# Kernel optimization log

Hardware: AMD Instinct MI355X
Metric: run time of the kernel (lower is better)

## Reference

```python
import jax, jax.numpy as jnp
import numpy as np

D_IN = 1024
D_OUT = 1024
N_HEADS = 16
D_K = D_OUT // N_HEADS
ROPE_THETA = 10000.0


def setup_inputs() -> dict:
    key = jax.random.key(0)
    ks = jax.random.split(key, 5)
    x = jax.random.normal(ks[0], (2, 2048, D_IN), dtype=jnp.float32)
    token_positions = jnp.arange(2048, dtype=jnp.int32)
    scale = 0.02
    wq = jax.random.normal(ks[1], (D_OUT, D_IN), dtype=jnp.float32) * scale
    wk = jax.random.normal(ks[2], (D_OUT, D_IN), dtype=jnp.float32) * scale
    wv = jax.random.normal(ks[3], (D_OUT, D_IN), dtype=jnp.float32) * scale
    wo = jax.random.normal(ks[4], (D_OUT, D_OUT), dtype=jnp.float32) * scale
    return {"x": x, "token_positions": token_positions, "wq": wq, "wk": wk, "wv": wv, "wo": wo}


def _rope(x, token_positions):
    # x: [..., S, d_k]; token_positions: [S]
    d_k = x.shape[-1]
    idx = jnp.arange(d_k)
    k = idx // 2
    # thetas[i, j] = pos_i / theta^(2*(j//2)/d_k)
    angles = token_positions[:, None].astype(x.dtype) / jnp.power(
        jnp.asarray(ROPE_THETA, x.dtype), 2.0 * k.astype(x.dtype) / d_k
    )  # [S, d_k]
    cos = jnp.cos(angles)
    sin = jnp.sin(angles) * jnp.where(idx % 2 == 0, -1.0, 1.0).astype(x.dtype)
    pair_swaps = idx + jnp.where(idx % 2 == 0, 1, -1)  # swap even/odd pairs
    return x * cos + x[..., pair_swaps] * sin


def _forward(x, token_positions, wq, wk, wv, wo):
    B, S, _ = x.shape
    # fused QKV projection (same math as concat + split)
    q = jnp.einsum("bsd,od->bso", x, wq)
    k = jnp.einsum("bsd,od->bso", x, wk)
    v = jnp.einsum("bsd,od->bso", x, wv)
    # split heads: [B, S, H*dk] -> [B, H, S, dk]
    split = lambda t: t.reshape(B, S, N_HEADS, D_K).transpose(0, 2, 1, 3)
    q, k, v = split(q), split(k), split(v)
    q = _rope(q, token_positions)
    k = _rope(k, token_positions)
    scores = jnp.einsum("bhqd,bhkd->bhqk", q, k) / jnp.sqrt(jnp.asarray(D_K, x.dtype))
    causal = jnp.tril(jnp.ones((S, S), dtype=bool))
    scores = jnp.where(causal, scores, -jnp.inf)
    probs = jax.nn.softmax(scores, axis=-1)
    ctx = jnp.einsum("bhqk,bhkd->bhqd", probs, v)
    merged = ctx.transpose(0, 2, 1, 3).reshape(B, S, D_OUT)
    return jnp.einsum("bsm,om->bso", merged, wo)


def reference(x, token_positions, wq, wk, wv, wo):
    return _forward(x, token_positions, wq, wk, wv, wo)
```

## Files before the change

### kernel.cpp

```cpp
#include <hip/hip_runtime.h>

#define D_MODEL 1024
#define SEQ     2048
#define BATCH   2
#define NHEADS  16
#define DK      64
#define NROWS   (BATCH*SEQ)

typedef unsigned short u16;
typedef __bf16 bf16x8 __attribute__((ext_vector_type(8)));
typedef float  f32x4  __attribute__((ext_vector_type(4)));

__device__ __forceinline__ u16 f2bf(float f) {
    union { float f; unsigned u; } v; v.f = f;
    unsigned u = v.u;
    u += 0x7fffu + ((u >> 16) & 1);
    return (u16)(u >> 16);
}
__device__ __forceinline__ float bf2f(u16 h) {
    union { unsigned u; float f; } v; v.u = ((unsigned)h) << 16;
    return v.f;
}
__device__ __forceinline__ unsigned cvtpk_bf16(float lo, float hi) {
    unsigned r;
    asm("v_cvt_pk_bf16_f32 %0, %1, %2" : "=v"(r) : "v"(lo), "v"(hi));
    return r;
}

__device__ __forceinline__ void gload_lds16(const u16* g, u16* l) {
    __builtin_amdgcn_global_load_lds(
        (const __attribute__((address_space(1))) void*)g,
        (__attribute__((address_space(3))) void*)l, 16, 0, 0);
}

__global__ void cvt_bf16_all(const float* __restrict__ x,
                             const float* __restrict__ w0, const float* __restrict__ w1,
                             const float* __restrict__ w2, const float* __restrict__ w3,
                             u16* __restrict__ xb, u16* __restrict__ wb) {
    int i = blockIdx.x * blockDim.x + threadIdx.x;
    int row = i >> 8;
    int c   = (i & 255) * 4;
    const float* src; u16* dst;
    if (row < 4096) {
        src = x + (size_t)row * 1024;
        dst = xb + (size_t)row * 1024;
    } else {
        int r2 = row - 4096;
        int ws = r2 >> 10;
        int rr = r2 & 1023;
        const float* wsrc = ws == 0 ? w0 : ws == 1 ? w1 : ws == 2 ? w2 : w3;
        src = wsrc + (size_t)rr * 1024;
        dst = wb + ((size_t)ws << 20) + (size_t)rr * 1024;
    }
    float4 v = *(const float4*)(src + c);
    uint2 o;
    o.x = (unsigned)f2bf(v.x) | ((unsigned)f2bf(v.y) << 16);
    o.y = (unsigned)f2bf(v.z) | ((unsigned)f2bf(v.w) << 16);
    *(uint2*)(dst + c) = o;
}

__global__ __launch_bounds__(256) void gemm_qkv_p(
    const u16* __restrict__ A, const u16* __restrict__ W,
    u16* __restrict__ Qp, u16* __restrict__ Kp, u16* __restrict__ Vt)
{
    __shared__ __align__(16) u16 Ash[128 * 32];
    __shared__ __align__(16) u16 Bsh[128 * 32];

    const int m0  = blockIdx.x * 128;
    const int sel = blockIdx.y >> 3;
    const int n0  = (blockIdx.y & 7) * 128;
    const u16* B = W + ((size_t)sel << 20);
    const int tid = threadIdx.x;
    const int lane = tid & 63;
    const int w    = tid >> 6;
    const int wr = w >> 1, wc = w & 1;
    const int fr = lane & 15;
    const int fk = (lane >> 4) * 8;
    const int rsub = lane >> 2;
    const int csub = (lane & 3) * 8;

    f32x4 acc[4][4];
#pragma unroll
    for (int i = 0; i < 4; ++i)
#pragma unroll
        for (int j = 0; j < 4; ++j) acc[i][j] = (f32x4){0.f, 0.f, 0.f, 0.f};

    for (int k0 = 0; k0 < 1024; k0 += 32) {
        __syncthreads();
        const u16* Ab = A + (size_t)(m0 + 16 * w + rsub) * 1024 + k0 + csub;
        const u16* Bb = B + (size_t)(n0 + 16 * w + rsub) * 1024 + k0 + csub;
#pragma unroll
        for (int half = 0; half < 2; ++half) {
            size_t ro = (size_t)(half * 64) * 1024;
            int lo = (half * 64 + 16 * w) * 32;
            gload_lds16(Ab + ro, &Ash[lo]);
            gload_lds16(Bb + ro, &Bsh[lo]);
        }
        __syncthreads();

        bf16x8 ah[4], bh[4];
#pragma unroll
        for (int i = 0; i < 4; ++i)
            ah[i] = *(const bf16x8*)&Ash[(wr * 64 + i * 16 + fr) * 32 + fk];
#pragma unroll
        for (int j = 0; j < 4; ++j)
            bh[j] = *(const bf16x8*)&Bsh[(wc * 64 + j * 16 + fr) * 32 + fk];
#pragma unroll
        for (int i = 0; i < 4; ++i)
#pragma unroll
            for (int j = 0; j < 4; ++j)
                acc[i][j] = __builtin_amdgcn_mfma_f32_16x16x32_bf16(ah[i], bh[j], acc[i][j], 0, 0, 0);
    }

    const int r0 = (lane >> 4) * 4;
#pragma unroll
    for (int i = 0; i < 4; ++i) {
#pragma unroll
        for (int j = 0; j < 4; ++j) {
            int col = n0 + wc * 64 + j * 16 + fr;
#pragma unroll
            for (int r = 0; r < 4; ++r) {
                int row = m0 + wr * 64 + i * 16 + r0 + r;
                u16 v = f2bf(acc[i][j][r]);
                if (sel == 0)      Qp[(size_t)row * 1024 + col] = v;
                else if (sel == 1) Kp[(size_t)row * 1024 + col] = v;
                else               Vt[(size_t)col * NROWS + row] = v;
            }
        }
    }
}

__global__ __launch_bounds__(256) void gemm_out_p(
    const u16* __restrict__ A, const u16* __restrict__ B, float* __restrict__ Cout)
{
    __shared__ __align__(16) u16 Ash[128 * 32];
    __shared__ __align__(16) u16 Bsh[128 * 32];

    const int m0 = blockIdx.x * 128;
    const int n0 = blockIdx.y * 128;
    const int tid = threadIdx.x;
    const int lane = tid & 63;
    const int w    = tid >> 6;
    const int wr = w >> 1, wc = w & 1;
    const int fr = lane & 15;
    const int fk = (lane >> 4) * 8;
    const int rsub = lane >> 2;
    const int csub = (lane & 3) * 8;

    f32x4 acc[4][4];
#pragma unroll
    for (int i = 0; i < 4; ++i)
#pragma unroll
        for (int j = 0; j < 4; ++j) acc[i][j] = (f32x4){0.f, 0.f, 0.f, 0.f};

    for (int k0 = 0; k0 < 1024; k0 += 32) {
        __syncthreads();
        const u16* Ab = A + (size_t)(m0 + 16 * w + rsub) * 1024 + k0 + csub;
        const u16* Bb = B + (size_t)(n0 + 16 * w + rsub) * 1024 + k0 + csub;
#pragma unroll
        for (int half = 0; half < 2; ++half) {
            size_t ro = (size_t)(half * 64) * 1024;
            int lo = (half * 64 + 16 * w) * 32;
            gload_lds16(Ab + ro, &Ash[lo]);
            gload_lds16(Bb + ro, &Bsh[lo]);
        }
        __syncthreads();

        bf16x8 ah[4], bh[4];
#pragma unroll
        for (int i = 0; i < 4; ++i)
            ah[i] = *(const bf16x8*)&Ash[(wr * 64 + i * 16 + fr) * 32 + fk];
#pragma unroll
        for (int j = 0; j < 4; ++j)
            bh[j] = *(const bf16x8*)&Bsh[(wc * 64 + j * 16 + fr) * 32 + fk];
#pragma unroll
        for (int i = 0; i < 4; ++i)
#pragma unroll
            for (int j = 0; j < 4; ++j)
                acc[i][j] = __builtin_amdgcn_mfma_f32_16x16x32_bf16(ah[i], bh[j], acc[i][j], 0, 0, 0);
    }

    const int r0 = (lane >> 4) * 4;
#pragma unroll
    for (int i = 0; i < 4; ++i) {
#pragma unroll
        for (int j = 0; j < 4; ++j) {
            int col = n0 + wc * 64 + j * 16 + fr;
#pragma unroll
            for (int r = 0; r < 4; ++r)
                Cout[(size_t)(m0 + wr * 64 + i * 16 + r0 + r) * 1024 + col] = acc[i][j][r];
        }
    }
}

__global__ void rope_plain(u16* __restrict__ qk, const int* __restrict__ pos) {
    int i = blockIdx.x * blockDim.x + threadIdx.x;
    int p = i & 511;
    int n = i >> 9;
    int s = n & 2047;
    int k = p & 31;
    int h = p >> 5;
    size_t base = (size_t)n * 1024 + h * DK + 2 * k;
    unsigned v = *(const unsigned*)&qk[base];
    float x0 = bf2f((u16)(v & 0xffff));
    float x1 = bf2f((u16)(v >> 16));
    float ang = (float)pos[s] * expf((float)k * -0.28782313662425575f);
    float c = cosf(ang), sn = sinf(ang);
    float qs = (n < 4096) ? 0.18033688011112042f : 1.0f;
    c *= qs; sn *= qs;
    float y0 = x0 * c - x1 * sn;
    float y1 = x1 * c + x0 * sn;
    *(unsigned*)&qk[base] = (unsigned)f2bf(y0) | ((unsigned)f2bf(y1) << 16);
}

__global__ __launch_bounds__(512, 4) void attn_v7(
    const u16* __restrict__ Qp, const u16* __restrict__ Kp, const u16* __restrict__ Vt,
    u16* __restrict__ Op, float* __restrict__ mlbuf)
{
    const int slot = 39 - (int)blockIdx.x;
    const int h = blockIdx.y, b = blockIdx.z;
    int g, rr;
    if (slot < 4)       { g = 0; rr = slot; }
    else if (slot < 12) { g = 1; rr = slot - 4; }
    else if (slot < 24) { g = 2; rr = slot - 12; }
    else                { g = 3; rr = slot - 24; }
    const int qq  = rr / (g + 1);
    const int qt2 = 4 * g + qq;
    const int c   = rr - qq * (g + 1);

    const int tid  = threadIdx.x;
    const int lane = tid & 63;
    const int w    = tid >> 6;
    const int fr = lane & 15;
    const int fg = lane >> 4;
    const int bS = b * SEQ;
    const int hd = h * DK;
    const int qbase = qt2 * 128 + 16 * w;
    const int ntk = 2 * qt2 + 2;
    const int kt0 = 8 * c;
    const int kt1 = min(8 * c + 8, ntk);

    __shared__ __align__(16) u16 Kl[2][64 * 64];
    __shared__ __align__(16) u16 Vl[2][64 * 64];
    __shared__ __align__(16) u16 Plds[8][16][72];

    const int srow = 8 * w + (lane >> 3);
    const int scol = (((lane & 7) ^ (lane >> 3)) * 8);
    const int swz  = (fr & 7) * 8;

    const u16* qrow = Qp + (size_t)(bS + qbase + fr) * 1024 + hd;
    bf16x8 qf0 = *(const bf16x8*)(qrow + fg * 8);
    bf16x8 qf1 = *(const bf16x8*)(qrow + 32 + fg * 8);

    f32x4 o[4];
#pragma unroll
    for (int j = 0; j < 4; ++j) o[j] = (f32x4){0.f, 0.f, 0.f, 0.f};
    float mrow = -1e30f, lrow = 0.f;

#define STAGE(BUF, KT) do { \
    int kb_ = (KT) * 64; \
    gload_lds16(Kp + (size_t)(bS + kb_ + srow) * 1024 + hd + scol, &Kl[BUF][(8 * w) * 64]); \
    gload_lds16(Vt + (size_t)(hd + srow) * NROWS + bS + kb_ + scol, &Vl[BUF][(8 * w) * 64]); \
} while (0)

    STAGE(0, kt0);
    __syncthreads();

    int cur = 0;
    for (int kt = kt0; kt < kt1; ++kt) {
        if (kt + 1 < kt1) STAGE(cur ^ 1, kt + 1);
        const int k0 = kt * 64;
        if (k0 <= qbase + 15) {
            bf16x8 kf[4][2];
#pragma unroll
            for (int t = 0; t < 4; ++t) {
                const u16* kr = &Kl[cur][(16 * t + fr) * 64];
                kf[t][0] = *(const bf16x8*)(kr + ((fg * 8) ^ swz));
                kf[t][1] = *(const bf16x8*)(kr + (((4 + fg) * 8) ^ swz));
            }
            f32x4 sc4[4];
#pragma unroll
            for (int t = 0; t < 4; ++t) {
                f32x4 a = (f32x4){0.f, 0.f, 0.f, 0.f};
                a = __builtin_amdgcn_mfma_f32_16x16x32_bf16(kf[t][0], qf0, a, 0, 0, 0);
                a = __builtin_amdgcn_mfma_f32_16x16x32_bf16(kf[t][1], qf1, a, 0, 0, 0);
                sc4[t] = a;
            }
            float p[4][4];
#pragma unroll
            for (int t = 0; t < 4; ++t)
#pragma unroll
                for (int r = 0; r < 4; ++r) p[t][r] = sc4[t][r];
            if (k0 + 63 > qbase) {
#pragma unroll
                for (int t = 0; t < 4; ++t)
#pragma unroll
                    for (int r = 0; r < 4; ++r)
                        if (k0 + 16 * t + 4 * fg + r > qbase + fr) p[t][r] = -1e30f;
            }
            float a0 = fmaxf(fmaxf(p[0][0], p[0][1]), fmaxf(p[0][2], p[0][3]));
            float a1 = fmaxf(fmaxf(p[1][0], p[1][1]), fmaxf(p[1][2], p[1][3]));
            float a2 = fmaxf(fmaxf(p[2][0], p[2][1]), fmaxf(p[2][2], p[2][3]));
            float a3 = fmaxf(fmaxf(p[3][0], p[3][1]), fmaxf(p[3][2], p[3][3]));
            float mx = fmaxf(fmaxf(a0, a1), fmaxf(a2, a3));
            mx = fmaxf(mx, __shfl_xor(mx, 16));
            mx = fmaxf(mx, __shfl_xor(mx, 32));
            float scf = 1.0f;
            if (!__all(mx <= mrow + 8.0f)) {
                float mnew = fmaxf(mrow, mx);
                scf = exp2f(mrow - mnew);
                float s0 = __shfl(scf, 4 * fg);
                float s1 = __shfl(scf, 4 * fg + 1);
                float s2 = __shfl(scf, 4 * fg + 2);
                float s3 = __shfl(scf, 4 * fg + 3);
#pragma unroll
                for (int j = 0; j < 4; ++j) {
                    o[j][0] *= s0; o[j][1] *= s1; o[j][2] *= s2; o[j][3] *= s3;
                }
                mrow = mnew;
            }
            float rs = 0.f;
#pragma unroll
            for (int t = 0; t < 4; ++t)
#pragma unroll
                for (int r = 0; r < 4; ++r) {
                    p[t][r] = exp2f(p[t][r] - mrow);
                    rs += p[t][r];
                }
            rs += __shfl_xor(rs, 16);
            rs += __shfl_xor(rs, 32);
            lrow = lrow * scf + rs;
#pragma unroll
            for (int t = 0; t < 4; ++t) {
                uint2 pk;
                pk.x = cvtpk_bf16(p[t][0], p[t][1]);
                pk.y = cvtpk_bf16(p[t][2], p[t][3]);
                *(uint2*)&Plds[w][fr][16 * t + 4 * fg] = pk;
            }
            bf16x8 pf0 = *(const bf16x8*)&Plds[w][fr][fg * 8];
            bf16x8 pf1 = *(const bf16x8*)&Plds[w][fr][32 + fg * 8];
#pragma unroll
            for (int j = 0; j < 4; ++j) {
                const u16* vr = &Vl[cur][(16 * j + fr) * 64];
                bf16x8 v0 = *(const bf16x8*)(vr + ((fg * 8) ^ swz));
                bf16x8 v1 = *(const bf16x8*)(vr + (((4 + fg) * 8) ^ swz));
                o[j] = __builtin_amdgcn_mfma_f32_16x16x32_bf16(pf0, v0, o[j], 0, 0, 0);
                o[j] = __builtin_amdgcn_mfma_f32_16x16x32_bf16(pf1, v1, o[j], 0, 0, 0);
            }
        }
        __syncthreads();
        cur ^= 1;
    }
#undef STAGE

    const int slotg = (b * NHEADS + h) * 40 + slot;
#pragma unroll
    for (int r = 0; r < 4; ++r) {
        int rrel = 16 * w + 4 * fg + r;
#pragma unroll
        for (int j = 0; j < 4; ++j)
            Op[((size_t)slotg * 128 + rrel) * 64 + 16 * j + fr] = f2bf(o[j][r]);
    }
    if (fg == 0) {
        float* pp = mlbuf + ((size_t)slotg * 128 + 16 * w + fr) * 2;
        pp[0] = mrow;
        pp[1] = lrow;
    }
}

__global__ void attn_combine3(const u16* __restrict__ Op, const float* __restrict__ mlbuf,
                              u16* __restrict__ Mb) {
    int i = blockIdx.x * blockDim.x + threadIdx.x;
    int row = i >> 7;
    int c8  = (i & 127) * 8;
    int h   = c8 >> 6;
    int s   = row & 2047;
    int b   = row >> 11;
    int qt2 = s >> 7;
    int g   = qt2 >> 2;
    int nch = g + 1;
    int slot0 = (b * NHEADS + h) * 40 + 2 * g * (g + 1) + (qt2 & 3) * (g + 1);
    int rrel = s & 127, crel = c8 & 63;

    float mv[4], lv[4];
    float m = -1e30f;
    for (int k = 0; k < nch; ++k) {
        const float* pp = mlbuf + ((size_t)(slot0 + k) * 128 + rrel) * 2;
        mv[k] = pp[0]; lv[k] = pp[1];
        m = fmaxf(m, mv[k]);
    }
    float L = 0.f;
    for (int k = 0; k < nch; ++k) {
        mv[k] = exp2f(mv[k] - m);
        L += lv[k] * mv[k];
    }
    float acc[8];
#pragma unroll
    for (int jj = 0; jj < 8; ++jj) acc[jj] = 0.f;
    for (int k = 0; k < nch; ++k) {
        float wgt = mv[k];
        uint4 u = *(const uint4*)(Op + ((size_t)(slot0 + k) * 128 + rrel) * 64 + crel);
        const unsigned* wrd = (const unsigned*)&u;
#pragma unroll
        for (int kk = 0; kk < 4; ++kk) {
            acc[2 * kk]     += wgt * bf2f((u16)(wrd[kk] & 0xffff));
            acc[2 * kk + 1] += wgt * bf2f((u16)(wrd[kk] >> 16));
        }
    }
    float inv = 1.0f / L;
    unsigned ou[4];
#pragma unroll
    for (int kk = 0; kk < 4; ++kk)
        ou[kk] = (unsigned)f2bf(acc[2 * kk] * inv) | ((unsigned)f2bf(acc[2 * kk + 1] * inv) << 16);
    *(uint4*)(Mb + (size_t)row * 1024 + c8) = *(uint4*)ou;
}

extern "C" void kernel_launch(void* const* d_in, const int* in_sizes, int n_in,
                              void* d_out, int out_size, void* d_ws, size_t ws_size,
                              hipStream_t stream) {
    const float* x   = (const float*)d_in[0];
    const int*   pos = (const int*)d_in[1];
    const float* wq  = (const float*)d_in[2];
    const float* wk  = (const float*)d_in[3];
    const float* wv  = (const float*)d_in[4];
    const float* wo  = (const float*)d_in[5];
    float* out = (float*)d_out;

    char* ws = (char*)d_ws;
    u16* xb  = (u16*)(ws);
    u16* wb  = (u16*)(ws + (24ull << 20));
    u16* wob = wb + 3 * (1 << 20);
    u16* Qp  = (u16*)(ws + (32ull << 20));
    u16* Kp  = (u16*)(ws + (40ull << 20));
    u16* Vt  = (u16*)(ws + (48ull << 20));
    u16* Mb  = (u16*)(ws + (56ull << 20));
    u16* Op  = (u16*)(ws);
    float* mlbuf = (float*)(ws + (21ull << 20));

    cvt_bf16_all<<<8192, 256, 0, stream>>>(x, wq, wk, wv, wo, xb, wb);

    gemm_qkv_p<<<dim3(NROWS / 128, 24), 256, 0, stream>>>(xb, wb, Qp, Kp, Vt);

    rope_plain<<<16384, 256, 0, stream>>>(Qp, pos);

    attn_v7<<<dim3(40, NHEADS, BATCH), 512, 0, stream>>>(Qp, Kp, Vt, Op, mlbuf);
    attn_combine3<<<2048, 256, 0, stream>>>(Op, mlbuf, Mb);

    gemm_out_p<<<dim3(NROWS / 128, 8), 256, 0, stream>>>(Mb, wob, out);
}
```

Measured before the change: 155.5 us.

## Stage K/V through registers with two-deep prefetch and raise MFMA priority

The attention kernel stops using direct global-to-LDS loads. Each K/V tile is now loaded into registers two iterations ahead and written to swizzled LDS one iteration ahead, which is meant to hide global latency behind the compute of the current tile. It also wraps the MFMA sections in s_setprio so matrix work gets scheduling priority, and raises the launch-bounds occupancy hint from 4 to 6. The costs are extra registers and VGPR-to-LDS store instructions, and the higher occupancy target may force register spills.

```diff
diff --git a/kernel.cpp b/kernel.cpp
--- a/kernel.cpp
+++ b/kernel.cpp
@@ -213,7 +213,7 @@
     *(unsigned*)&qk[base] = (unsigned)f2bf(y0) | ((unsigned)f2bf(y1) << 16);
 }
 
-__global__ __launch_bounds__(512, 4) void attn_v7(
+__global__ __launch_bounds__(512, 6) void attn_v8(
     const u16* __restrict__ Qp, const u16* __restrict__ Kp, const u16* __restrict__ Vt,
     u16* __restrict__ Op, float* __restrict__ mlbuf)
 {
@@ -244,9 +244,10 @@
     __shared__ __align__(16) u16 Vl[2][64 * 64];
     __shared__ __align__(16) u16 Plds[8][16][72];
 
-    const int srow = 8 * w + (lane >> 3);
-    const int scol = (((lane & 7) ^ (lane >> 3)) * 8);
-    const int swz  = (fr & 7) * 8;
+    const int dsrow  = 8 * w + (lane >> 3);
+    const int lincol = (lane & 7) * 8;
+    const int dsoff  = dsrow * 64 + (((lane & 7) ^ (lane >> 3)) * 8);
+    const int swz    = (fr & 7) * 8;
 
     const u16* qrow = Qp + (size_t)(bS + qbase + fr) * 1024 + hd;
     bf16x8 qf0 = *(const bf16x8*)(qrow + fg * 8);
@@ -257,18 +258,27 @@
     for (int j = 0; j < 4; ++j) o[j] = (f32x4){0.f, 0.f, 0.f, 0.f};
     float mrow = -1e30f, lrow = 0.f;
 
-#define STAGE(BUF, KT) do { \
-    int kb_ = (KT) * 64; \
-    gload_lds16(Kp + (size_t)(bS + kb_ + srow) * 1024 + hd + scol, &Kl[BUF][(8 * w) * 64]); \
-    gload_lds16(Vt + (size_t)(hd + srow) * NROWS + bS + kb_ + scol, &Vl[BUF][(8 * w) * 64]); \
+    uint4 kreg, vreg;
+#define LOADR(KT) do { \
+    kreg = *(const uint4*)(Kp + (size_t)(bS + (KT) * 64 + dsrow) * 1024 + hd + lincol); \
+    vreg = *(const uint4*)(Vt + (size_t)(hd + dsrow) * NROWS + bS + (KT) * 64 + lincol); \
 } while (0)
-
-    STAGE(0, kt0);
+#define DSW(BUF) do { \
+    *(uint4*)&Kl[BUF][dsoff] = kreg; \
+    *(uint4*)&Vl[BUF][dsoff] = vreg; \
+} while (0)
+
+    LOADR(kt0);
+    DSW(0);
+    if (kt0 + 1 < kt1) LOADR(kt0 + 1);
     __syncthreads();
 
     int cur = 0;
     for (int kt = kt0; kt < kt1; ++kt) {
-        if (kt + 1 < kt1) STAGE(cur ^ 1, kt + 1);
+        if (kt + 1 < kt1) {
+            DSW(cur ^ 1);
+            if (kt + 2 < kt1) LOADR(kt + 2);
+        }
         const int k0 = kt * 64;
         if (k0 <= qbase + 15) {
             bf16x8 kf[4][2];
@@ -279,6 +289,7 @@
                 kf[t][1] = *(const bf16x8*)(kr + (((4 + fg) * 8) ^ swz));
             }
             f32x4 sc4[4];
+            __builtin_amdgcn_s_setprio(1);
 #pragma unroll
             for (int t = 0; t < 4; ++t) {
                 f32x4 a = (f32x4){0.f, 0.f, 0.f, 0.f};
@@ -286,6 +297,7 @@
                 a = __builtin_amdgcn_mfma_f32_16x16x32_bf16(kf[t][1], qf1, a, 0, 0, 0);
                 sc4[t] = a;
             }
+            __builtin_amdgcn_s_setprio(0);
             float p[4][4];
 #pragma unroll
             for (int t = 0; t < 4; ++t)
@@ -339,6 +351,7 @@
             }
             bf16x8 pf0 = *(const bf16x8*)&Plds[w][fr][fg * 8];
             bf16x8 pf1 = *(const bf16x8*)&Plds[w][fr][32 + fg * 8];
+            __builtin_amdgcn_s_setprio(1);
 #pragma unroll
             for (int j = 0; j < 4; ++j) {
                 const u16* vr = &Vl[cur][(16 * j + fr) * 64];
@@ -347,11 +360,13 @@
                 o[j] = __builtin_amdgcn_mfma_f32_16x16x32_bf16(pf0, v0, o[j], 0, 0, 0);
                 o[j] = __builtin_amdgcn_mfma_f32_16x16x32_bf16(pf1, v1, o[j], 0, 0, 0);
             }
+            __builtin_amdgcn_s_setprio(0);
         }
         __syncthreads();
         cur ^= 1;
     }
-#undef STAGE
+#undef LOADR
+#undef DSW
 
     const int slotg = (b * NHEADS + h) * 40 + slot;
 #pragma unroll
@@ -443,7 +458,7 @@
 
     rope_plain<<<16384, 256, 0, stream>>>(Qp, pos);
 
-    attn_v7<<<dim3(40, NHEADS, BATCH), 512, 0, stream>>>(Qp, Kp, Vt, Op, mlbuf);
+    attn_v8<<<dim3(40, NHEADS, BATCH), 512, 0, stream>>>(Qp, Kp, Vt, Op, mlbuf);
     attn_combine3<<<2048, 256, 0, stream>>>(Op, mlbuf, Mb);
 
     gemm_out_p<<<dim3(NROWS / 128, 8), 256, 0, stream>>>(Mb, wob, out);
```

After: 183.2 us. 1.18x slower.
